# Performance work log

Measured on AMD Instinct MI355X. Metric: run time of the kernel, lower is better.

The kernel has to match this reference:

```python
import jax, jax.numpy as jnp
import numpy as np
from jax import lax


def _gru_layer(x_seq, W, U, b, units):
    """Keras GRU (reset_after=True, gate order [z, r, h]) with activation=relu.
    x_seq: (B, T, F). Returns (ys (B,T,units), h_last (B,units))."""
    b_in, b_rec = b[0], b[1]                      # each (3*units,)
    # Precompute all input projections once: (B, T, 3*units)
    x_proj = jnp.einsum('btf,fj->btj', x_seq, W) + b_in
    B = x_seq.shape[0]
    h0 = jnp.zeros((B, units), dtype=x_seq.dtype)

    def step(h, xp_t):
        rec = h @ U + b_rec                        # (B, 3*units)
        zr = jax.nn.sigmoid(xp_t[:, :2 * units] + rec[:, :2 * units])
        z, r = zr[:, :units], zr[:, units:]
        hh = jax.nn.relu(xp_t[:, 2 * units:] + r * rec[:, 2 * units:])
        h_new = z * h + (1.0 - z) * hh
        return h_new, h_new

    h_last, ys = lax.scan(step, h0, jnp.swapaxes(x_proj, 0, 1))  # scan over T
    return jnp.swapaxes(ys, 0, 1), h_last


def setup_inputs() -> dict:
    key = jax.random.key(0)
    ks = jax.random.split(key, 6)
    B, T, F, U1, U2 = 64, 2048, 15, 256, 256
    s = lambda fan_in: 1.0 / np.sqrt(fan_in)
    return {
        'input_data': jax.random.normal(ks[0], (B, T, F), dtype=jnp.float32),
        'W1': jax.random.normal(ks[1], (F, 3 * U1), dtype=jnp.float32) * s(F),
        'U1': jax.random.normal(ks[2], (U1, 3 * U1), dtype=jnp.float32) * s(U1),
        'b1': jnp.zeros((2, 3 * U1), dtype=jnp.float32),
        'W2': jax.random.normal(ks[3], (U1, 3 * U2), dtype=jnp.float32) * s(U1),
        'U2': jax.random.normal(ks[4], (U2, 3 * U2), dtype=jnp.float32) * s(U2),
        'b2': jnp.zeros((2, 3 * U2), dtype=jnp.float32),
    }


def reference(input_data, W1, U1, b1, W2, U2, b2):
    u1 = U1.shape[0]
    u2 = U2.shape[0]
    seq1, state1 = _gru_layer(input_data, W1, U1, b1, u1)  # gru1: return_sequences + state
    seq2, state2 = _gru_layer(seq1, W2, U2, b2, u2)        # gru2: last output + state
    x = seq2[:, -1, :]                                      # last output (== state2)
    return (x, state1, state2)
```

## Files before the change

kernel.cpp:

```cpp
#include <hip/hip_runtime.h>

#define BB 64
#define TT 2048
#define FF 15
#define UU 256
#define N3 768

typedef _Float16 half8 __attribute__((ext_vector_type(8)));
typedef float f32x4 __attribute__((ext_vector_type(4)));

__device__ float g_seq1[BB * TT * UU];
__device__ float g_xp[(size_t)BB * TT * N3];
__device__ uint4 g_U1p[48 * 8 * 64];
__device__ uint4 g_U2p[48 * 8 * 64];

__global__ __launch_bounds__(256) void prep_upk(const float* __restrict__ U,
                                                unsigned* __restrict__ Up) {
    int idx = blockIdx.x * 256 + threadIdx.x;
    int d = idx & 3, l = (idx >> 2) & 63, kt = (idx >> 8) & 7, nt = idx >> 11;
    int row = kt * 32 + ((l >> 4) << 3) + 2 * d;
    int col = nt * 16 + (l & 15);
    unsigned short lo = __builtin_bit_cast(unsigned short, (_Float16)U[row * N3 + col]);
    unsigned short hi = __builtin_bit_cast(unsigned short, (_Float16)U[(row + 1) * N3 + col]);
    Up[idx] = (unsigned)lo | ((unsigned)hi << 16);
}

__global__ __launch_bounds__(256) void gemm_k15(
    const float* __restrict__ x, const float* __restrict__ W1,
    const float* __restrict__ bin, float* __restrict__ C) {
    __shared__ float xr[8][FF];
    const int m0 = blockIdx.x * 8;
    const int j  = blockIdx.y * 256 + threadIdx.x;
    if (threadIdx.x < 8 * FF) {
        int r = threadIdx.x / FF, k = threadIdx.x - r * FF;
        xr[r][k] = x[(size_t)(m0 + r) * FF + k];
    }
    __syncthreads();
    float wv[FF];
#pragma unroll
    for (int k = 0; k < FF; k++) wv[k] = W1[k * N3 + j];
    const float bj = bin[j];
#pragma unroll
    for (int r = 0; r < 8; r++) {
        float a = bj;
#pragma unroll
        for (int k = 0; k < FF; k++) a += xr[r][k] * wv[k];
        C[(size_t)(m0 + r) * N3 + j] = a;
    }
}

__global__ __launch_bounds__(256) void gemm_xp(
    const float* __restrict__ A, const float* __restrict__ Bw,
    const float* __restrict__ bin, float* __restrict__ C) {
    __shared__ float As[16][64];
    __shared__ float Bs[16][64];
    const int tid = threadIdx.x;
    const int m0 = blockIdx.x * 64, n0 = blockIdx.y * 64;
    const int tm = (tid & 15) * 4;
    const int tn = (tid >> 4) * 4;
    float acc[4][4] = {};
    const int lm = tid >> 2, lk = (tid & 3) * 4;
    const int lkb = tid >> 4, ln = (tid & 15) * 4;
    for (int k0 = 0; k0 < 256; k0 += 16) {
        float4 av = *(const float4*)&A[(size_t)(m0 + lm) * 256 + k0 + lk];
        float4 bv = *(const float4*)&Bw[(size_t)(k0 + lkb) * N3 + n0 + ln];
        As[lk + 0][lm] = av.x; As[lk + 1][lm] = av.y;
        As[lk + 2][lm] = av.z; As[lk + 3][lm] = av.w;
        *(float4*)&Bs[lkb][ln] = bv;
        __syncthreads();
#pragma unroll
        for (int kk = 0; kk < 16; kk++) {
            float4 a = *(const float4*)&As[kk][tm];
            float4 b = *(const float4*)&Bs[kk][tn];
            acc[0][0] += a.x * b.x; acc[0][1] += a.x * b.y; acc[0][2] += a.x * b.z; acc[0][3] += a.x * b.w;
            acc[1][0] += a.y * b.x; acc[1][1] += a.y * b.y; acc[1][2] += a.y * b.z; acc[1][3] += a.y * b.w;
            acc[2][0] += a.z * b.x; acc[2][1] += a.z * b.y; acc[2][2] += a.z * b.z; acc[2][3] += a.z * b.w;
            acc[3][0] += a.w * b.x; acc[3][1] += a.w * b.y; acc[3][2] += a.w * b.z; acc[3][3] += a.w * b.w;
        }
        __syncthreads();
    }
#pragma unroll
    for (int i = 0; i < 4; i++) {
        float4 o = make_float4(acc[i][0] + bin[n0 + tn + 0], acc[i][1] + bin[n0 + tn + 1],
                               acc[i][2] + bin[n0 + tn + 2], acc[i][3] + bin[n0 + tn + 3]);
        *(float4*)&C[(size_t)(m0 + tm + i) * N3 + n0 + tn] = o;
    }
}

__global__ __launch_bounds__(512) __attribute__((amdgpu_waves_per_eu(2, 2)))
void gru_mfma2(const uint4* __restrict__ Up, const float* __restrict__ brec,
               const float* __restrict__ xp, float* __restrict__ seq_out,
               float* __restrict__ state_out, float* __restrict__ extra_out) {
    const int b = blockIdx.x, tid = threadIdx.x;
    const int w = tid >> 6, lane = tid & 63;
    const int l15 = lane & 15;
    const int uA = 32 * w + l15;
    const int uB = uA + 16;

    __shared__ __align__(16) _Float16 h2s[2][UU];

    const int tz = 2 * w, tr = 16 + 2 * w, th = 32 + 2 * w;
    half8 ub[48];
#pragma unroll
    for (int kt = 0; kt < 8; kt++) {
        ub[0 * 8 + kt] = __builtin_bit_cast(half8, Up[((tz + 0) * 8 + kt) * 64 + lane]);
        ub[1 * 8 + kt] = __builtin_bit_cast(half8, Up[((tz + 1) * 8 + kt) * 64 + lane]);
        ub[2 * 8 + kt] = __builtin_bit_cast(half8, Up[((tr + 0) * 8 + kt) * 64 + lane]);
        ub[3 * 8 + kt] = __builtin_bit_cast(half8, Up[((tr + 1) * 8 + kt) * 64 + lane]);
        ub[4 * 8 + kt] = __builtin_bit_cast(half8, Up[((th + 0) * 8 + kt) * 64 + lane]);
        ub[5 * 8 + kt] = __builtin_bit_cast(half8, Up[((th + 1) * 8 + kt) * 64 + lane]);
    }
    const float brzA = brec[uA], brrA = brec[uA + UU], brhA = brec[uA + 2 * UU];
    const float brzB = brec[uB], brrB = brec[uB + UU], brhB = brec[uB + 2 * UU];

    if (tid < 128) ((unsigned*)h2s[0])[tid] = 0u;
    float hA = 0.f, hB = 0.f;
    __syncthreads();

    const float* __restrict__ xpb = xp + (size_t)b * TT * N3;
    float xzA = xpb[uA], xrA = xpb[uA + UU], xhA = xpb[uA + 2 * UU];
    float xzB = xpb[uB], xrB = xpb[uB + UU], xhB = xpb[uB + 2 * UU];

    const int arow = (lane >> 4) << 3;

    for (int t = 0; t < TT; t++) {
        const float* xn = xpb + (size_t)(t + 1 < TT ? t + 1 : t) * N3;
        float xzAn = xn[uA], xrAn = xn[uA + UU], xhAn = xn[uA + 2 * UU];
        float xzBn = xn[uB], xrBn = xn[uB + UU], xhBn = xn[uB + 2 * UU];

        const _Float16* hcur = h2s[t & 1];
        f32x4 a0 = {0.f, 0.f, 0.f, 0.f}, a1 = a0, a2 = a0, a3 = a0, a4 = a0, a5 = a0;
#pragma unroll
        for (int kt = 0; kt < 8; kt++) {
            half8 av = *(const half8*)&hcur[kt * 32 + arow];
            a0 = __builtin_amdgcn_mfma_f32_16x16x32_f16(av, ub[0 * 8 + kt], a0, 0, 0, 0);
            a1 = __builtin_amdgcn_mfma_f32_16x16x32_f16(av, ub[1 * 8 + kt], a1, 0, 0, 0);
            a2 = __builtin_amdgcn_mfma_f32_16x16x32_f16(av, ub[2 * 8 + kt], a2, 0, 0, 0);
            a3 = __builtin_amdgcn_mfma_f32_16x16x32_f16(av, ub[3 * 8 + kt], a3, 0, 0, 0);
            a4 = __builtin_amdgcn_mfma_f32_16x16x32_f16(av, ub[4 * 8 + kt], a4, 0, 0, 0);
            a5 = __builtin_amdgcn_mfma_f32_16x16x32_f16(av, ub[5 * 8 + kt], a5, 0, 0, 0);
        }

        float zA = 1.f / (1.f + __expf(-(xzA + a0[0] + brzA)));
        float zB = 1.f / (1.f + __expf(-(xzB + a1[0] + brzB)));
        float rA = 1.f / (1.f + __expf(-(xrA + a2[0] + brrA)));
        float rB = 1.f / (1.f + __expf(-(xrB + a3[0] + brrB)));
        float hhA = xhA + rA * (a4[0] + brhA); hhA = hhA > 0.f ? hhA : 0.f;
        float hhB = xhB + rB * (a5[0] + brhB); hhB = hhB > 0.f ? hhB : 0.f;
        hA = zA * hA + (1.f - zA) * hhA;
        hB = zB * hB + (1.f - zB) * hhB;

        _Float16* hnxt = h2s[(t + 1) & 1];
        if (lane < 32) {
            int   u  = (lane < 16) ? uA : uB;
            float hv = (lane < 16) ? hA : hB;
            hnxt[u] = (_Float16)hv;
            if (seq_out)
                seq_out[(size_t)b * TT * UU + (size_t)t * UU + u] = hv;
        }
        __syncthreads();
        xzA = xzAn; xrA = xrAn; xhA = xhAn;
        xzB = xzBn; xrB = xrBn; xhB = xhBn;
    }

    if (lane < 32) {
        int   u  = (lane < 16) ? uA : uB;
        float hv = (lane < 16) ? hA : hB;
        state_out[b * UU + u] = hv;
        if (extra_out) extra_out[b * UU + u] = hv;
    }
}

extern "C" void kernel_launch(void* const* d_in, const int* in_sizes, int n_in,
                              void* d_out, int out_size, void* d_ws, size_t ws_size,
                              hipStream_t stream) {
    const float* x  = (const float*)d_in[0];
    const float* W1 = (const float*)d_in[1];
    const float* U1 = (const float*)d_in[2];
    const float* b1 = (const float*)d_in[3];
    const float* W2 = (const float*)d_in[4];
    const float* U2 = (const float*)d_in[5];
    const float* b2 = (const float*)d_in[6];
    float* out = (float*)d_out;

    uint4* U1p; hipGetSymbolAddress((void**)&U1p, HIP_SYMBOL(g_U1p));
    uint4* U2p; hipGetSymbolAddress((void**)&U2p, HIP_SYMBOL(g_U2p));
    float* seq1; hipGetSymbolAddress((void**)&seq1, HIP_SYMBOL(g_seq1));
    float* xp;   hipGetSymbolAddress((void**)&xp,   HIP_SYMBOL(g_xp));

    prep_upk<<<384, 256, 0, stream>>>(U1, (unsigned*)U1p);
    prep_upk<<<384, 256, 0, stream>>>(U2, (unsigned*)U2p);

    gemm_k15<<<dim3(BB * TT / 8, 3), 256, 0, stream>>>(x, W1, b1, xp);
    gru_mfma2<<<BB, 512, 0, stream>>>(U1p, b1 + N3, xp, seq1, out + BB * UU, nullptr);

    gemm_xp<<<dim3(BB * TT / 64, N3 / 64), 256, 0, stream>>>(seq1, W2, b2, xp);
    gru_mfma2<<<BB, 512, 0, stream>>>(U2p, b2 + N3, xp, nullptr, out + 2 * BB * UU, out);
}
```

Before: 5.268 ms.

## Replace FP32 layer-2 input projection GEMM with fp16 MFMA kernel

The layer-2 input projection (131072x256 by 256x768) moves from a scalar FP32 shared-memory tiled GEMM to an MFMA 16x16x32 fp16 kernel. W2 is pre-packed into the MFMA B-fragment layout, and activations are converted to fp16 on load. Each block handles 64 rows and all 768 columns across 8 waves with 24 accumulators each. This lowers FMA cost at the price of fp16 rounding of seq1 and W2, high register pressure, and uncoalesced strided output stores.

After: 5.026 ms. 1.05x faster.

```diff
diff --git a/kernel.cpp b/kernel.cpp
--- a/kernel.cpp
+++ b/kernel.cpp
@@ -13,6 +13,7 @@
 __device__ float g_xp[(size_t)BB * TT * N3];
 __device__ uint4 g_U1p[48 * 8 * 64];
 __device__ uint4 g_U2p[48 * 8 * 64];
+__device__ uint4 g_W2p[48 * 8 * 64];
 
 __global__ __launch_bounds__(256) void prep_upk(const float* __restrict__ U,
                                                 unsigned* __restrict__ Up) {
@@ -49,41 +50,42 @@
     }
 }
 
-__global__ __launch_bounds__(256) void gemm_xp(
-    const float* __restrict__ A, const float* __restrict__ Bw,
+__global__ __launch_bounds__(512) void gemm_xp_mfma(
+    const float* __restrict__ A, const uint4* __restrict__ Wp,
     const float* __restrict__ bin, float* __restrict__ C) {
-    __shared__ float As[16][64];
-    __shared__ float Bs[16][64];
-    const int tid = threadIdx.x;
-    const int m0 = blockIdx.x * 64, n0 = blockIdx.y * 64;
-    const int tm = (tid & 15) * 4;
-    const int tn = (tid >> 4) * 4;
-    float acc[4][4] = {};
-    const int lm = tid >> 2, lk = (tid & 3) * 4;
-    const int lkb = tid >> 4, ln = (tid & 15) * 4;
-    for (int k0 = 0; k0 < 256; k0 += 16) {
-        float4 av = *(const float4*)&A[(size_t)(m0 + lm) * 256 + k0 + lk];
-        float4 bv = *(const float4*)&Bw[(size_t)(k0 + lkb) * N3 + n0 + ln];
-        As[lk + 0][lm] = av.x; As[lk + 1][lm] = av.y;
-        As[lk + 2][lm] = av.z; As[lk + 3][lm] = av.w;
-        *(float4*)&Bs[lkb][ln] = bv;
-        __syncthreads();
-#pragma unroll
-        for (int kk = 0; kk < 16; kk++) {
-            float4 a = *(const float4*)&As[kk][tm];
-            float4 b = *(const float4*)&Bs[kk][tn];
-            acc[0][0] += a.x * b.x; acc[0][1] += a.x * b.y; acc[0][2] += a.x * b.z; acc[0][3] += a.x * b.w;
-            acc[1][0] += a.y * b.x; acc[1][1] += a.y * b.y; acc[1][2] += a.y * b.z; acc[1][3] += a.y * b.w;
-            acc[2][0] += a.z * b.x; acc[2][1] += a.z * b.y; acc[2][2] += a.z * b.z; acc[2][3] += a.z * b.w;
-            acc[3][0] += a.w * b.x; acc[3][1] += a.w * b.y; acc[3][2] += a.w * b.z; acc[3][3] += a.w * b.w;
+    const int tid = threadIdx.x, w = tid >> 6, lane = tid & 63;
+    const int mt = w >> 1;
+    const int nb = (w & 1) * 24;
+    const int arow = blockIdx.x * 64 + mt * 16 + (lane & 15);
+    const int ko   = (lane >> 4) * 8;
+
+    f32x4 acc[24] = {};
+    const float* ap = A + (size_t)arow * 256 + ko;
+
+#pragma unroll
+    for (int kt = 0; kt < 8; kt++) {
+        float4 p0 = *(const float4*)(ap + kt * 32);
+        float4 p1 = *(const float4*)(ap + kt * 32 + 4);
+        half8 av;
+        av[0] = (_Float16)p0.x; av[1] = (_Float16)p0.y;
+        av[2] = (_Float16)p0.z; av[3] = (_Float16)p0.w;
+        av[4] = (_Float16)p1.x; av[5] = (_Float16)p1.y;
+        av[6] = (_Float16)p1.z; av[7] = (_Float16)p1.w;
+        const uint4* wp = Wp + (size_t)(nb * 8 + kt) * 64 + lane;
+#pragma unroll
+        for (int n = 0; n < 24; n++) {
+            half8 bf = __builtin_bit_cast(half8, wp[(size_t)n * 8 * 64]);
+            acc[n] = __builtin_amdgcn_mfma_f32_16x16x32_f16(av, bf, acc[n], 0, 0, 0);
         }
-        __syncthreads();
-    }
-#pragma unroll
-    for (int i = 0; i < 4; i++) {
-        float4 o = make_float4(acc[i][0] + bin[n0 + tn + 0], acc[i][1] + bin[n0 + tn + 1],
-                               acc[i][2] + bin[n0 + tn + 2], acc[i][3] + bin[n0 + tn + 3]);
-        *(float4*)&C[(size_t)(m0 + tm + i) * N3 + n0 + tn] = o;
+    }
+    const int rbase = blockIdx.x * 64 + mt * 16 + (lane >> 4) * 4;
+#pragma unroll
+    for (int n = 0; n < 24; n++) {
+        int col = (nb + n) * 16 + (lane & 15);
+        float bv = bin[col];
+#pragma unroll
+        for (int d = 0; d < 4; d++)
+            C[(size_t)(rbase + d) * N3 + col] = acc[n][d] + bv;
     }
 }
 
@@ -94,8 +96,7 @@
     const int b = blockIdx.x, tid = threadIdx.x;
     const int w = tid >> 6, lane = tid & 63;
     const int l15 = lane & 15;
-    const int uA = 32 * w + l15;
-    const int uB = uA + 16;
+    const int uA = 32 * w + l15, uB = uA + 16;
 
     __shared__ __align__(16) _Float16 h2s[2][UU];
 
@@ -185,15 +186,17 @@
 
     uint4* U1p; hipGetSymbolAddress((void**)&U1p, HIP_SYMBOL(g_U1p));
     uint4* U2p; hipGetSymbolAddress((void**)&U2p, HIP_SYMBOL(g_U2p));
+    uint4* W2p; hipGetSymbolAddress((void**)&W2p, HIP_SYMBOL(g_W2p));
     float* seq1; hipGetSymbolAddress((void**)&seq1, HIP_SYMBOL(g_seq1));
     float* xp;   hipGetSymbolAddress((void**)&xp,   HIP_SYMBOL(g_xp));
 
     prep_upk<<<384, 256, 0, stream>>>(U1, (unsigned*)U1p);
     prep_upk<<<384, 256, 0, stream>>>(U2, (unsigned*)U2p);
+    prep_upk<<<384, 256, 0, stream>>>(W2, (unsigned*)W2p);
 
     gemm_k15<<<dim3(BB * TT / 8, 3), 256, 0, stream>>>(x, W1, b1, xp);
     gru_mfma2<<<BB, 512, 0, stream>>>(U1p, b1 + N3, xp, seq1, out + BB * UU, nullptr);
 
-    gemm_xp<<<dim3(BB * TT / 64, N3 / 64), 256, 0, stream>>>(seq1, W2, b2, xp);
+    gemm_xp_mfma<<<BB * TT / 64, 512, 0, stream>>>(seq1, W2p, b2, xp);
     gru_mfma2<<<BB, 512, 0, stream>>>(U2p, b2 + N3, xp, nullptr, out + 2 * BB * UU, out);
 }
```
